# Kernel tuning notes

Hardware: AMD Instinct MI355X
Metric: run time of the kernel (lower is better)

The kernel has to match this reference:

```python
import jax, jax.numpy as jnp
import numpy as np

EMBED = 2048
NUM_HEADS = 32
HEAD_DIM = EMBED // NUM_HEADS  # 64 (original head dim; sets the scaling)
RANK_KQ = 1024
RANK_V = 1024
DK = RANK_KQ // NUM_HEADS  # 32 low-rank kq head dim
DV = RANK_V // NUM_HEADS   # 32 low-rank v head dim
B, S = 2, 2048


def setup_inputs() -> dict:
    key = jax.random.key(0)
    ks = jax.random.split(key, 10)
    std = 0.02
    hidden_states = jax.random.normal(ks[0], (B, S, EMBED), dtype=jnp.float32)
    # causal additive mask, shape (B, 1, S, S) as asserted in forward
    neg = jnp.finfo(jnp.float32).min
    causal = jnp.where(jnp.tril(jnp.ones((S, S), dtype=bool)), 0.0, neg)
    attention_mask = jnp.broadcast_to(causal[None, None], (B, 1, S, S)).astype(jnp.float32)
    Wq = jax.random.normal(ks[1], (RANK_KQ, EMBED), dtype=jnp.float32) * std
    bq = jax.random.normal(ks[2], (RANK_KQ,), dtype=jnp.float32) * std
    Wk = jax.random.normal(ks[3], (RANK_KQ, EMBED), dtype=jnp.float32) * std
    bk = jax.random.normal(ks[4], (RANK_KQ,), dtype=jnp.float32) * std
    Wv = jax.random.normal(ks[5], (RANK_V, EMBED), dtype=jnp.float32) * std
    bv = jax.random.normal(ks[6], (RANK_V,), dtype=jnp.float32) * std
    Wo = jax.random.normal(ks[7], (EMBED, RANK_V), dtype=jnp.float32) * std
    bo = jax.random.normal(ks[8], (EMBED,), dtype=jnp.float32) * std
    return {"hidden_states": hidden_states, "attention_mask": attention_mask,
            "Wq": Wq, "bq": bq, "Wk": Wk, "bk": bk, "Wv": Wv, "bv": bv,
            "Wo": Wo, "bo": bo}


def reference(hidden_states, attention_mask, Wq, bq, Wk, bk, Wv, bv, Wo, bo):
    bsz, tgt_len, _ = hidden_states.shape
    scaling = HEAD_DIM ** (-0.5)  # uses ORIGINAL head_dim, not low-rank dim

    def split_heads(x, d):  # (b, s, H*d) -> (b, H, s, d)
        return x.reshape(bsz, -1, NUM_HEADS, d).transpose(0, 2, 1, 3)

    q = split_heads((hidden_states @ Wq.T + bq) * scaling, DK)
    k = split_heads(hidden_states @ Wk.T + bk, DK)
    v = split_heads(hidden_states @ Wv.T + bv, DV)

    # scores: (b, H, tgt, src)
    attn = jnp.einsum('bhqd,bhkd->bhqk', q, k)
    attn = attn + attention_mask  # broadcast over heads
    attn = jnp.maximum(attn, jnp.finfo(attn.dtype).min)
    attn = jax.nn.softmax(attn, axis=-1)

    out = jnp.einsum('bhqk,bhkd->bhqd', attn, v)  # (b, H, tgt, DV)
    out = out.transpose(0, 2, 1, 3).reshape(bsz, tgt_len, RANK_V)
    return out @ Wo.T + bo
```

## Files before the change

### kernel.cpp

```cpp
#include <hip/hip_runtime.h>
#include <stdint.h>

typedef __attribute__((ext_vector_type(8))) short bf16x8;
typedef __attribute__((ext_vector_type(4))) float f32x4;
typedef unsigned short ushort_t;

#define AS1 __attribute__((address_space(1)))
#define AS3 __attribute__((address_space(3)))

static __device__ __forceinline__ ushort_t f2b(float f) {
    union { float f; unsigned u; } x; x.f = f;
    unsigned r = x.u + 0x7fffu + ((x.u >> 16) & 1u);
    return (ushort_t)(r >> 16);
}
static __device__ __forceinline__ f32x4 mfma16(bf16x8 a, bf16x8 b, f32x4 c) {
    return __builtin_amdgcn_mfma_f32_16x16x32_bf16(a, b, c, 0, 0, 0);
}
static __device__ __forceinline__ void gl_lds16(const ushort_t* g, ushort_t* l) {
    __builtin_amdgcn_global_load_lds((const AS1 void*)g, (AS3 void*)l, 16, 0, 0);
}
static __device__ __forceinline__ unsigned pk2(float a, float b) {
    unsigned r;
    asm("v_cvt_pk_bf16_f32 %0, %1, %2" : "=v"(r) : "v"(a), "v"(b));
    return r;
}

__global__ __launch_bounds__(256)
void cvt_bf16(const float* __restrict__ s, ushort_t* __restrict__ d, int n8)
{
    int i = blockIdx.x * 256 + threadIdx.x;
    if (i >= n8) return;
    const float* p = s + (size_t)i * 8;
    f32x4 a = *(const f32x4*)p;
    f32x4 b = *(const f32x4*)(p + 4);
    bf16x8 r;
#pragma unroll
    for (int j = 0; j < 4; ++j) { r[j] = (short)f2b(a[j]); r[j+4] = (short)f2b(b[j]); }
    *(bf16x8*)(d + (size_t)i * 8) = r;
}

__global__ __launch_bounds__(256)
void cvt_w3(const float* __restrict__ wq, const float* __restrict__ wk,
            const float* __restrict__ wv, ushort_t* __restrict__ d)
{
    const float* s = (blockIdx.y == 0) ? wq : (blockIdx.y == 1) ? wk : wv;
    ushort_t* dst = d + (size_t)blockIdx.y * 2097152;
    int i = blockIdx.x * 256 + threadIdx.x;
    const float* p = s + (size_t)i * 8;
    f32x4 a = *(const f32x4*)p;
    f32x4 b = *(const f32x4*)(p + 4);
    bf16x8 r;
#pragma unroll
    for (int j = 0; j < 4; ++j) { r[j] = (short)f2b(a[j]); r[j+4] = (short)f2b(b[j]); }
    *(bf16x8*)(dst + (size_t)i * 8) = r;
}

__global__ __launch_bounds__(256, 3)
void gemm_p2(const ushort_t* __restrict__ A, const ushort_t* __restrict__ B,
             const float* __restrict__ b0, const float* __restrict__ b1,
             const float* __restrict__ b2, void* __restrict__ Cv,
             int M, int N, int K, float scale, int epi)
{
    __shared__ __align__(16) ushort_t lds[24576];
    const int tid = threadIdx.x;
    const int wave = tid >> 6, lane = tid & 63;
    const int l16 = lane & 15, quad = lane >> 4;
    const int bm = blockIdx.x * 128, bn = blockIdx.y * 128;
    const int wm = (wave >> 1) * 64, wn = (wave & 1) * 64;
    const int xo = (l16 & 8) << 1;
    const int NT = K >> 5;

    f32x4 acc[4][4];
#pragma unroll
    for (int i = 0; i < 4; ++i)
#pragma unroll
        for (int j = 0; j < 4; ++j) acc[i][j] = (f32x4){0.f, 0.f, 0.f, 0.f};

    auto stg = [&](int sl, int rp) {
        int ko = sl << 5;
#pragma unroll
        for (int call = 0; call < 2; ++call) {
            int c = call * 256 + tid;
            int cl = c ^ (((c >> 5) & 1) << 1);
            int row = cl >> 2, c8 = cl & 3;
            gl_lds16(A + (size_t)(bm + row) * K + ko + c8 * 8,
                     lds + rp * 8192 + c * 8);
            gl_lds16(B + (size_t)(bn + row) * K + ko + c8 * 8,
                     lds + rp * 8192 + 4096 + c * 8);
        }
    };

    stg(0, 0);
    stg(1, 1);
    asm volatile("s_waitcnt vmcnt(4)" ::: "memory");
    __builtin_amdgcn_s_barrier();

    int ra = 0, rs = 2;
    for (int s = 0; s < NT; ++s) {
        if (s + 2 < NT) stg(s + 2, rs);
        bf16x8 af[4], bfr[4];
#pragma unroll
        for (int i = 0; i < 4; ++i)
            af[i] = *(const bf16x8*)(lds + ra * 8192
                      + (wm + i * 16 + l16) * 32 + ((quad * 8) ^ xo));
#pragma unroll
        for (int j = 0; j < 4; ++j)
            bfr[j] = *(const bf16x8*)(lds + ra * 8192 + 4096
                      + (wn + j * 16 + l16) * 32 + ((quad * 8) ^ xo));
        asm volatile("s_waitcnt lgkmcnt(0)" ::: "memory");
        __builtin_amdgcn_sched_barrier(0);
        __builtin_amdgcn_s_setprio(1);
#pragma unroll
        for (int i = 0; i < 4; ++i)
#pragma unroll
            for (int j = 0; j < 4; ++j)
                acc[i][j] = mfma16(af[i], bfr[j], acc[i][j]);
        __builtin_amdgcn_s_setprio(0);
        if (s == NT - 2) asm volatile("s_waitcnt vmcnt(0)" ::: "memory");
        else             asm volatile("s_waitcnt vmcnt(4)" ::: "memory");
        __builtin_amdgcn_s_barrier();
        ra = (ra == 2) ? 0 : ra + 1;
        rs = (rs == 2) ? 0 : rs + 1;
    }

#pragma unroll
    for (int i = 0; i < 4; ++i) {
#pragma unroll
        for (int j = 0; j < 4; ++j) {
            int col = bn + wn + j * 16 + l16;
            if (epi == 0) {
                float bvs = b0[col];
#pragma unroll
                for (int r = 0; r < 4; ++r) {
                    int row = bm + wm + i * 16 + quad * 4 + r;
                    ((float*)Cv)[(size_t)row * N + col] = (acc[i][j][r] + bvs) * scale;
                }
            } else {
                int mat = col >> 10, nc = col & 1023;
                const float* bp = (mat == 0) ? b0 : (mat == 1) ? b1 : b2;
                float bvs = bp[nc];
                int h = nc >> 5, d = nc & 31;
                if (mat == 2) {
                    int row0 = bm + wm + i * 16 + quad * 4;
                    int b = row0 >> 11, s2 = row0 & 2047;
                    ushort_t* dst = (ushort_t*)Cv + (size_t)2 * 4194304
                                  + ((size_t)(b * 32 + h) * 32 + d) * 2048 + s2;
                    uint2 w;
                    w.x = ((unsigned)f2b(acc[i][j][1] + bvs) << 16) | f2b(acc[i][j][0] + bvs);
                    w.y = ((unsigned)f2b(acc[i][j][3] + bvs) << 16) | f2b(acc[i][j][2] + bvs);
                    *(uint2*)dst = w;
                } else {
                    float sc = (mat == 0) ? 0.125f : 1.0f;
                    ushort_t* dst = (ushort_t*)Cv + (size_t)mat * 4194304;
#pragma unroll
                    for (int r = 0; r < 4; ++r) {
                        int row = bm + wm + i * 16 + quad * 4 + r;
                        int b = row >> 11, s2 = row & 2047;
                        float v = (acc[i][j][r] + bvs) * sc;
                        dst[(((size_t)(b * 32 + h) * 2048 + s2) << 5) + d] = f2b(v);
                    }
                }
            }
        }
    }
}

__global__ __launch_bounds__(512, 1)
void gemm8b(const ushort_t* __restrict__ A, const ushort_t* __restrict__ B,
            const float* __restrict__ bias, float* __restrict__ C,
            int M, int N, int K, float scale)
{
    __shared__ __align__(16) ushort_t lds[49152];
    const int tid = threadIdx.x;
    const int wave = tid >> 6, lane = tid & 63;
    const int l16 = lane & 15, quad = lane >> 4;
    const int wr = wave >> 2, wc = wave & 3;
    const int bm = blockIdx.x * 128, bn = blockIdx.y * 256;
    const int xo = (l16 & 8) << 1;
    const int S = K >> 4;
    const int NT = K >> 7;

    f32x4 acc[4][4];
#pragma unroll
    for (int i = 0; i < 4; ++i)
#pragma unroll
        for (int j = 0; j < 4; ++j) acc[i][j] = (f32x4){0.f,0.f,0.f,0.f};

    auto stg = [&](int s_) {
        int r = s_ & 7;
        ushort_t* ldst = lds + (r >> 1) * 12288 + (r & 1) * 8192;
        int ko = (s_ >> 1) << 5;
        if (s_ & 1) {
            int c = tid;
            int cl = c ^ (((c >> 5) & 1) << 1);
            gl_lds16(A + (size_t)(bm + (cl >> 2)) * K + ko + (cl & 3) * 8,
                     ldst + c * 8);
        } else {
#pragma unroll
            for (int call = 0; call < 2; ++call) {
                int c = call * 512 + tid;
                int cl = c ^ (((c >> 5) & 1) << 1);
                gl_lds16(B + (size_t)(bn + (cl >> 2)) * K + ko + (cl & 3) * 8,
                         ldst + c * 8);
            }
        }
    };

#pragma unroll
    for (int s0 = 0; s0 < 7; ++s0) stg(s0);
    asm volatile("s_waitcnt vmcnt(5)" ::: "memory");
    __builtin_amdgcn_s_barrier();

    for (int t = 0; t < NT; ++t) {
        const bool lastit = (t == NT - 1);
        bf16x8 bfr[4], af[2];
#pragma unroll
        for (int p = 0; p < 8; ++p) {
            asm volatile("" ::: "memory");
            const int offB = (p >> 1) * 12288;
            const int offA = offB + 8192;
            if ((p & 1) == 0) {
#pragma unroll
                for (int j = 0; j < 4; ++j)
                    bfr[j] = *(const bf16x8*)(lds + offB
                              + (wc * 64 + j * 16 + l16) * 32 + ((quad * 8) ^ xo));
            }
#pragma unroll
            for (int m = 0; m < 2; ++m)
                af[m] = *(const bf16x8*)(lds + offA
                          + (wr * 64 + (p & 1) * 32 + m * 16 + l16) * 32
                          + ((quad * 8) ^ xo));
            { int s_ = 8 * t + 7 + p; if (s_ < S) stg(s_); }
            __builtin_amdgcn_s_barrier();
            asm volatile("s_waitcnt lgkmcnt(0)" ::: "memory");
            __builtin_amdgcn_sched_barrier(0);
            __builtin_amdgcn_s_setprio(1);
#pragma unroll
            for (int m = 0; m < 2; ++m)
#pragma unroll
                for (int j = 0; j < 4; ++j)
                    acc[(p & 1) * 2 + m][j] =
                        mfma16(af[m], bfr[j], acc[(p & 1) * 2 + m][j]);
            __builtin_amdgcn_s_setprio(0);
            if (p == 3) {
                if (lastit) asm volatile("s_waitcnt vmcnt(0)" ::: "memory");
                else        asm volatile("s_waitcnt vmcnt(5)" ::: "memory");
            } else if (p == 7) {
                if (!lastit) asm volatile("s_waitcnt vmcnt(5)" ::: "memory");
            }
            __builtin_amdgcn_s_barrier();
        }
    }

#pragma unroll
    for (int i = 0; i < 4; ++i) {
#pragma unroll
        for (int j = 0; j < 4; ++j) {
            int col = bn + wc * 64 + j * 16 + l16;
            float bvs = bias[col];
#pragma unroll
            for (int r = 0; r < 4; ++r) {
                int row = bm + wr * 64 + i * 16 + quad * 4 + r;
                C[(size_t)row * N + col] = (acc[i][j][r] + bvs) * scale;
            }
        }
    }
}

__global__ __launch_bounds__(256, 4)
void attn(const ushort_t* __restrict__ Q, const ushort_t* __restrict__ Kg,
          const ushort_t* __restrict__ VT, ushort_t* __restrict__ Ctx)
{
    __shared__ __align__(16) ushort_t Ps[4][32 * 72];
    const int tid = threadIdx.x, wave = tid >> 6, lane = tid & 63;
    const int l16 = lane & 15, quad = lane >> 4, quad4 = quad * 4;
    const int bh = blockIdx.x;
    const int pr = blockIdx.y;
    const ushort_t* Qh = Q  + (size_t)bh * 2048 * 32;
    const ushort_t* Kh = Kg + (size_t)bh * 2048 * 32;
    const ushort_t* Vh = VT + (size_t)bh * 32 * 2048;
    const int b = bh >> 5, h = bh & 31;
    ushort_t* P0 = &Ps[wave][0];

    for (int half = 0; half < 2; ++half) {
        const int qt = half ? (15 - pr) : pr;
        const int q0 = qt * 128 + wave * 32;

        bf16x8 qf0 = *(const bf16x8*)(Qh + (size_t)(q0 + l16) * 32 + quad * 8);
        bf16x8 qf1 = *(const bf16x8*)(Qh + (size_t)(q0 + 16 + l16) * 32 + quad * 8);

        f32x4 o00 = (f32x4){0.f,0.f,0.f,0.f}, o01 = o00, o10 = o00, o11 = o00;
        float rs0 = 0.f, rs1 = 0.f;

        const int nchw = ((q0 + 31) >> 6) + 1;
        for (int c = 0; c < nchw; ++c) {
            const int kv0 = c * 64;
            bf16x8 kf[4];
#pragma unroll
            for (int t = 0; t < 4; ++t)
                kf[t] = *(const bf16x8*)(Kh + (size_t)(kv0 + t * 16 + l16) * 32 + quad * 8);
            f32x4 st0[4], st1[4];
#pragma unroll
            for (int t = 0; t < 4; ++t) {
                st0[t] = mfma16(kf[t], qf0, (f32x4){0.f,0.f,0.f,0.f});
                st1[t] = mfma16(kf[t], qf1, (f32x4){0.f,0.f,0.f,0.f});
            }
            bf16x8 vA0 = *(const bf16x8*)(Vh + (size_t)l16 * 2048 + kv0 + quad * 8);
            bf16x8 vA1 = *(const bf16x8*)(Vh + (size_t)l16 * 2048 + kv0 + 32 + quad * 8);
            bf16x8 vB0 = *(const bf16x8*)(Vh + (size_t)(16 + l16) * 2048 + kv0 + quad * 8);
            bf16x8 vB1 = *(const bf16x8*)(Vh + (size_t)(16 + l16) * 2048 + kv0 + 32 + quad * 8);

            const int qk0 = q0 + l16 - kv0;
            auto softmax_pack = [&](bool masked) {
#pragma unroll
                for (int t = 0; t < 4; ++t) {
                    float p0[4], p1[4];
#pragma unroll
                    for (int r = 0; r < 4; ++r) {
                        const int kk = t * 16 + quad4 + r;
                        float e0 = __expf(st0[t][r]);
                        float e1 = __expf(st1[t][r]);
                        p0[r] = (!masked || kk <= qk0)      ? e0 : 0.f;
                        p1[r] = (!masked || kk <= qk0 + 16) ? e1 : 0.f;
                        rs0 += p0[r]; rs1 += p1[r];
                    }
                    uint2 w0, w1;
                    w0.x = pk2(p0[0], p0[1]); w0.y = pk2(p0[2], p0[3]);
                    w1.x = pk2(p1[0], p1[1]); w1.y = pk2(p1[2], p1[3]);
                    *(uint2*)(P0 + (size_t)l16 * 72 + t * 16 + quad4) = w0;
                    *(uint2*)(P0 + (size_t)(16 + l16) * 72 + t * 16 + quad4) = w1;
                }
            };
            if (kv0 + 63 <= q0) softmax_pack(false); else softmax_pack(true);

            asm volatile("s_waitcnt lgkmcnt(0)" ::: "memory");
#pragma unroll
            for (int ks = 0; ks < 2; ++ks) {
                bf16x8 pa0 = *(const bf16x8*)(P0 + (size_t)l16 * 72 + ks * 32 + quad * 8);
                bf16x8 pa1 = *(const bf16x8*)(P0 + (size_t)(16 + l16) * 72 + ks * 32 + quad * 8);
                bf16x8 va = ks ? vA1 : vA0;
                bf16x8 vb = ks ? vB1 : vB0;
                o00 = mfma16(pa0, va, o00);
                o01 = mfma16(pa0, vb, o01);
                o10 = mfma16(pa1, va, o10);
                o11 = mfma16(pa1, vb, o11);
            }
        }

        rs0 += __shfl_xor(rs0, 16); rs0 += __shfl_xor(rs0, 32);
        rs1 += __shfl_xor(rs1, 16); rs1 += __shfl_xor(rs1, 32);

#pragma unroll
        for (int r = 0; r < 4; ++r) {
            const int qr = q0 + quad4 + r;
            float inv0 = 1.0f / __shfl(rs0, quad4 + r);
            float inv1 = 1.0f / __shfl(rs1, quad4 + r);
            size_t base0 = ((size_t)b * 2048 + qr) * 1024 + h * 32;
            size_t base1 = ((size_t)b * 2048 + qr + 16) * 1024 + h * 32;
            Ctx[base0 + l16]      = f2b(o00[r] * inv0);
            Ctx[base0 + 16 + l16] = f2b(o01[r] * inv0);
            Ctx[base1 + l16]      = f2b(o10[r] * inv1);
            Ctx[base1 + 16 + l16] = f2b(o11[r] * inv1);
        }
    }
}

extern "C" void kernel_launch(void* const* d_in, const int* in_sizes, int n_in,
                              void* d_out, int out_size, void* d_ws, size_t ws_size,
                              hipStream_t stream)
{
    const float* H  = (const float*)d_in[0];
    const float* Wq = (const float*)d_in[2];
    const float* bq = (const float*)d_in[3];
    const float* Wk = (const float*)d_in[4];
    const float* bk = (const float*)d_in[5];
    const float* Wv = (const float*)d_in[6];
    const float* bv = (const float*)d_in[7];
    const float* Wo = (const float*)d_in[8];
    const float* bo = (const float*)d_in[9];

    ushort_t* Hb   = (ushort_t*)d_ws;
    ushort_t* Wcat = Hb   + (size_t)8388608;
    ushort_t* Qb   = Wcat + (size_t)6291456;
    ushort_t* Kb   = Qb   + (size_t)4194304;
    ushort_t* Vtb  = Kb   + (size_t)4194304;
    ushort_t* Ctx  = Vtb  + (size_t)4194304;
    ushort_t* Wob  = Hb;

    dim3 blk(256, 1, 1);
    hipLaunchKernelGGL(cvt_bf16, dim3(4096, 1, 1), blk, 0, stream, H, Hb, 1048576);
    hipLaunchKernelGGL(cvt_w3, dim3(1024, 3, 1), blk, 0, stream, Wq, Wk, Wv, Wcat);

    hipLaunchKernelGGL(gemm_p2, dim3(32, 24, 1), blk, 0, stream,
                       Hb, Wcat, bq, bk, bv, (void*)Qb, 4096, 3072, 2048, 1.0f, 2);

    hipLaunchKernelGGL(cvt_bf16, dim3(1024, 1, 1), blk, 0, stream, Wo, Wob, 262144);

    hipLaunchKernelGGL(attn, dim3(64, 8, 1), blk, 0, stream, Qb, Kb, Vtb, Ctx);

    hipLaunchKernelGGL(gemm8b, dim3(32, 8, 1), dim3(512, 1, 1), 0, stream,
                       Ctx, Wob, bo, (float*)d_out, 4096, 2048, 1024, 1.0f);
}
```

Baseline: 282.5 us.

## Replace QKV projection GEMM with 512-thread 128x384 tile and deep LDS pipeline

```diff
diff --git a/kernel.cpp b/kernel.cpp
--- a/kernel.cpp
+++ b/kernel.cpp
@@ -55,110 +55,121 @@
     *(bf16x8*)(dst + (size_t)i * 8) = r;
 }
 
-__global__ __launch_bounds__(256, 3)
-void gemm_p2(const ushort_t* __restrict__ A, const ushort_t* __restrict__ B,
-             const float* __restrict__ b0, const float* __restrict__ b1,
-             const float* __restrict__ b2, void* __restrict__ Cv,
-             int M, int N, int K, float scale, int epi)
-{
-    __shared__ __align__(16) ushort_t lds[24576];
+__global__ __launch_bounds__(512, 1)
+void gemm8c(const ushort_t* __restrict__ A, const ushort_t* __restrict__ B,
+            const float* __restrict__ b0, const float* __restrict__ b1,
+            const float* __restrict__ b2, void* __restrict__ Cv,
+            int M, int N, int K)
+{
+    __shared__ __align__(16) ushort_t lds[65536];
     const int tid = threadIdx.x;
     const int wave = tid >> 6, lane = tid & 63;
     const int l16 = lane & 15, quad = lane >> 4;
-    const int bm = blockIdx.x * 128, bn = blockIdx.y * 128;
-    const int wm = (wave >> 1) * 64, wn = (wave & 1) * 64;
+    const int wr = wave >> 2, wc = wave & 3;
+    const int bm = blockIdx.x * 128, bn = blockIdx.y * 384;
     const int xo = (l16 & 8) << 1;
-    const int NT = K >> 5;
-
-    f32x4 acc[4][4];
+    const int S = K >> 4;
+    const int NT = K >> 7;
+
+    f32x4 acc[4][6];
 #pragma unroll
     for (int i = 0; i < 4; ++i)
 #pragma unroll
-        for (int j = 0; j < 4; ++j) acc[i][j] = (f32x4){0.f, 0.f, 0.f, 0.f};
-
-    auto stg = [&](int sl, int rp) {
-        int ko = sl << 5;
-#pragma unroll
-        for (int call = 0; call < 2; ++call) {
-            int c = call * 256 + tid;
+        for (int j = 0; j < 6; ++j) acc[i][j] = (f32x4){0.f,0.f,0.f,0.f};
+
+    auto stg = [&](int s_) {
+        int slot = s_ & 7;
+        ushort_t* base = lds + (slot >> 1) * 16384;
+        int ko = (s_ >> 1) << 5;
+        if (s_ & 1) {
+            int c = tid;
             int cl = c ^ (((c >> 5) & 1) << 1);
-            int row = cl >> 2, c8 = cl & 3;
-            gl_lds16(A + (size_t)(bm + row) * K + ko + c8 * 8,
-                     lds + rp * 8192 + c * 8);
-            gl_lds16(B + (size_t)(bn + row) * K + ko + c8 * 8,
-                     lds + rp * 8192 + 4096 + c * 8);
+            gl_lds16(A + (size_t)(bm + (cl >> 2)) * K + ko + (cl & 3) * 8,
+                     base + 12288 + c * 8);
+        } else {
+#pragma unroll
+            for (int call = 0; call < 3; ++call) {
+                int c = call * 512 + tid;
+                int cl = c ^ (((c >> 5) & 1) << 1);
+                gl_lds16(B + (size_t)(bn + (cl >> 2)) * K + ko + (cl & 3) * 8,
+                         base + c * 8);
+            }
         }
     };
 
-    stg(0, 0);
-    stg(1, 1);
-    asm volatile("s_waitcnt vmcnt(4)" ::: "memory");
+#pragma unroll
+    for (int s0 = 0; s0 < 7; ++s0) stg(s0);
+    asm volatile("s_waitcnt vmcnt(7)" ::: "memory");
     __builtin_amdgcn_s_barrier();
 
-    int ra = 0, rs = 2;
-    for (int s = 0; s < NT; ++s) {
-        if (s + 2 < NT) stg(s + 2, rs);
-        bf16x8 af[4], bfr[4];
-#pragma unroll
-        for (int i = 0; i < 4; ++i)
-            af[i] = *(const bf16x8*)(lds + ra * 8192
-                      + (wm + i * 16 + l16) * 32 + ((quad * 8) ^ xo));
-#pragma unroll
-        for (int j = 0; j < 4; ++j)
-            bfr[j] = *(const bf16x8*)(lds + ra * 8192 + 4096
-                      + (wn + j * 16 + l16) * 32 + ((quad * 8) ^ xo));
-        asm volatile("s_waitcnt lgkmcnt(0)" ::: "memory");
-        __builtin_amdgcn_sched_barrier(0);
-        __builtin_amdgcn_s_setprio(1);
-#pragma unroll
-        for (int i = 0; i < 4; ++i)
-#pragma unroll
-            for (int j = 0; j < 4; ++j)
-                acc[i][j] = mfma16(af[i], bfr[j], acc[i][j]);
-        __builtin_amdgcn_s_setprio(0);
-        if (s == NT - 2) asm volatile("s_waitcnt vmcnt(0)" ::: "memory");
-        else             asm volatile("s_waitcnt vmcnt(4)" ::: "memory");
-        __builtin_amdgcn_s_barrier();
-        ra = (ra == 2) ? 0 : ra + 1;
-        rs = (rs == 2) ? 0 : rs + 1;
+    for (int t = 0; t < NT; ++t) {
+        const bool lastit = (t == NT - 1);
+        bf16x8 bfr[6], af[2];
+#pragma unroll
+        for (int p = 0; p < 8; ++p) {
+            asm volatile("" ::: "memory");
+            const int offB = (p >> 1) * 16384;
+            const int offA = offB + 12288;
+            if ((p & 1) == 0) {
+#pragma unroll
+                for (int j = 0; j < 6; ++j)
+                    bfr[j] = *(const bf16x8*)(lds + offB
+                              + (wc * 96 + j * 16 + l16) * 32 + ((quad * 8) ^ xo));
+            }
+#pragma unroll
+            for (int m = 0; m < 2; ++m)
+                af[m] = *(const bf16x8*)(lds + offA
+                          + (wr * 64 + (p & 1) * 32 + m * 16 + l16) * 32
+                          + ((quad * 8) ^ xo));
+            { int s_ = 8 * t + 7 + p; if (s_ < S) stg(s_); }
+            __builtin_amdgcn_s_barrier();
+            asm volatile("s_waitcnt lgkmcnt(0)" ::: "memory");
+            __builtin_amdgcn_sched_barrier(0);
+            __builtin_amdgcn_s_setprio(1);
+#pragma unroll
+            for (int m = 0; m < 2; ++m)
+#pragma unroll
+                for (int j = 0; j < 6; ++j)
+                    acc[(p & 1) * 2 + m][j] =
+                        mfma16(af[m], bfr[j], acc[(p & 1) * 2 + m][j]);
+            __builtin_amdgcn_s_setprio(0);
+            if (p == 3) {
+                if (lastit) asm volatile("s_waitcnt vmcnt(0)" ::: "memory");
+                else        asm volatile("s_waitcnt vmcnt(7)" ::: "memory");
+            } else if (p == 7) {
+                if (!lastit) asm volatile("s_waitcnt vmcnt(7)" ::: "memory");
+            }
+            __builtin_amdgcn_s_barrier();
+        }
     }
 
 #pragma unroll
     for (int i = 0; i < 4; ++i) {
 #pragma unroll
-        for (int j = 0; j < 4; ++j) {
-            int col = bn + wn + j * 16 + l16;
-            if (epi == 0) {
-                float bvs = b0[col];
+        for (int j = 0; j < 6; ++j) {
+            int col = bn + wc * 96 + j * 16 + l16;
+            int mat = col >> 10, nc = col & 1023;
+            const float* bp = (mat == 0) ? b0 : (mat == 1) ? b1 : b2;
+            float bvs = bp[nc];
+            int h = nc >> 5, d = nc & 31;
+            if (mat == 2) {
+                int row0 = bm + wr * 64 + i * 16 + quad * 4;
+                int b = row0 >> 11, s2 = row0 & 2047;
+                ushort_t* dst = (ushort_t*)Cv + (size_t)2 * 4194304
+                              + ((size_t)(b * 32 + h) * 32 + d) * 2048 + s2;
+                uint2 w;
+                w.x = ((unsigned)f2b(acc[i][j][1] + bvs) << 16) | f2b(acc[i][j][0] + bvs);
+                w.y = ((unsigned)f2b(acc[i][j][3] + bvs) << 16) | f2b(acc[i][j][2] + bvs);
+                *(uint2*)dst = w;
+            } else {
+                float sc = (mat == 0) ? 0.125f : 1.0f;
+                ushort_t* dst = (ushort_t*)Cv + (size_t)mat * 4194304;
 #pragma unroll
                 for (int r = 0; r < 4; ++r) {
-                    int row = bm + wm + i * 16 + quad * 4 + r;
-                    ((float*)Cv)[(size_t)row * N + col] = (acc[i][j][r] + bvs) * scale;
-                }
-            } else {
-                int mat = col >> 10, nc = col & 1023;
-                const float* bp = (mat == 0) ? b0 : (mat == 1) ? b1 : b2;
-                float bvs = bp[nc];
-                int h = nc >> 5, d = nc & 31;
-                if (mat == 2) {
-                    int row0 = bm + wm + i * 16 + quad * 4;
-                    int b = row0 >> 11, s2 = row0 & 2047;
-                    ushort_t* dst = (ushort_t*)Cv + (size_t)2 * 4194304
-                                  + ((size_t)(b * 32 + h) * 32 + d) * 2048 + s2;
-                    uint2 w;
-                    w.x = ((unsigned)f2b(acc[i][j][1] + bvs) << 16) | f2b(acc[i][j][0] + bvs);
-                    w.y = ((unsigned)f2b(acc[i][j][3] + bvs) << 16) | f2b(acc[i][j][2] + bvs);
-                    *(uint2*)dst = w;
-                } else {
-                    float sc = (mat == 0) ? 0.125f : 1.0f;
-                    ushort_t* dst = (ushort_t*)Cv + (size_t)mat * 4194304;
-#pragma unroll
-                    for (int r = 0; r < 4; ++r) {
-                        int row = bm + wm + i * 16 + quad * 4 + r;
-                        int b = row >> 11, s2 = row & 2047;
-                        float v = (acc[i][j][r] + bvs) * sc;
-                        dst[(((size_t)(b * 32 + h) * 2048 + s2) << 5) + d] = f2b(v);
-                    }
+                    int row = bm + wr * 64 + i * 16 + quad * 4 + r;
+                    int b = row >> 11, s2 = row & 2047;
+                    float v = (acc[i][j][r] + bvs) * sc;
+                    dst[(((size_t)(b * 32 + h) * 2048 + s2) << 5) + d] = f2b(v);
                 }
             }
         }
@@ -391,8 +402,8 @@
     hipLaunchKernelGGL(cvt_bf16, dim3(4096, 1, 1), blk, 0, stream, H, Hb, 1048576);
     hipLaunchKernelGGL(cvt_w3, dim3(1024, 3, 1), blk, 0, stream, Wq, Wk, Wv, Wcat);
 
-    hipLaunchKernelGGL(gemm_p2, dim3(32, 24, 1), blk, 0, stream,
-                       Hb, Wcat, bq, bk, bv, (void*)Qb, 4096, 3072, 2048, 1.0f, 2);
+    hipLaunchKernelGGL(gemm8c, dim3(32, 8, 1), dim3(512, 1, 1), 0, stream,
+                       Hb, Wcat, bq, bk, bv, (void*)Qb, 4096, 3072, 2048);
 
     hipLaunchKernelGGL(cvt_bf16, dim3(1024, 1, 1), blk, 0, stream, Wo, Wob, 262144);
 
```

New measurement: 275.9 us. 2.3% less time.
